# Performance work log

Measured on AMD Instinct MI355X. Metric: run time of the kernel, lower is better.

The kernel has to match this reference:

```python
import jax, jax.numpy as jnp
import numpy as np

N = 50000        # nodes
E = 1600000      # edges
G = 512          # graphs in batch
IN = 128         # in_dim
HID = 32         # hidden_dim
H = 4            # heads in conv1
NEG_SLOPE = 0.2  # PyG GATConv default


def setup_inputs() -> dict:
    key = jax.random.key(0)
    ks = jax.random.split(key, 20)
    s = 0.05
    return {
        "x": jax.random.normal(ks[0], (N, IN), jnp.float32),
        "edge_index": jax.random.randint(ks[1], (2, E), 0, N, dtype=jnp.int64),
        "edge_attr": jax.random.normal(ks[2], (E, 8), jnp.float32),
        "batch": jnp.sort(jax.random.randint(ks[3], (N,), 0, G, dtype=jnp.int64)),
        # conv1: in=IN, out=HID, heads=H, concat=True
        "W1": jax.random.normal(ks[4], (IN, H * HID), jnp.float32) * s,
        "a_src1": jax.random.normal(ks[5], (H, HID), jnp.float32) * s,
        "a_dst1": jax.random.normal(ks[6], (H, HID), jnp.float32) * s,
        "b1": jnp.zeros((H * HID,), jnp.float32),
        # conv2: in=H*HID, out=HID, heads=1, concat=False
        "W2": jax.random.normal(ks[7], (H * HID, HID), jnp.float32) * s,
        "a_src2": jax.random.normal(ks[8], (1, HID), jnp.float32) * s,
        "a_dst2": jax.random.normal(ks[9], (1, HID), jnp.float32) * s,
        "b2": jnp.zeros((HID,), jnp.float32),
        # classifier: HID -> HID//2 -> 1
        "Wc1": jax.random.normal(ks[10], (HID, HID // 2), jnp.float32) * s,
        "bc1": jnp.zeros((HID // 2,), jnp.float32),
        "Wc2": jax.random.normal(ks[11], (HID // 2, 1), jnp.float32) * s,
        "bc2": jnp.zeros((1,), jnp.float32),
    }


def gat_layer(x, src, dst, W, a_src, a_dst, b, heads, ch, concat, n):
    """PyG GATConv (eval mode): linear, edge-gathered additive attention,
    per-destination segment softmax, scatter-add aggregation."""
    h = (x @ W).reshape(n, heads, ch)                       # [N,H,C]
    alpha_s = jnp.sum(h * a_src, axis=-1)                   # [N,H]
    alpha_d = jnp.sum(h * a_dst, axis=-1)                   # [N,H]
    e = jax.nn.leaky_relu(alpha_s[src] + alpha_d[dst], NEG_SLOPE)  # [Etot,H]
    m = jax.lax.stop_gradient(jax.ops.segment_max(e, dst, num_segments=n))
    ex = jnp.exp(e - m[dst])
    den = jax.ops.segment_sum(ex, dst, num_segments=n)      # [N,H]
    alpha = ex / den[dst]                                   # [Etot,H]
    out = jax.ops.segment_sum(alpha[:, :, None] * h[src], dst, num_segments=n)
    out = out.reshape(n, heads * ch) if concat else out.mean(axis=1)
    return out + b


def reference(x, edge_index, edge_attr, batch,
              W1, a_src1, a_dst1, b1,
              W2, a_src2, a_dst2, b2,
              Wc1, bc1, Wc2, bc2):
    # add self-loops (PyG GATConv default)
    loop = jnp.arange(N, dtype=edge_index.dtype)
    src = jnp.concatenate([edge_index[0], loop])
    dst = jnp.concatenate([edge_index[1], loop])

    h = jax.nn.elu(gat_layer(x, src, dst, W1, a_src1, a_dst1, b1, H, HID, True, N))
    h = jax.nn.elu(gat_layer(h, src, dst, W2, a_src2, a_dst2, b2, 1, HID, False, N))

    # global mean pool over graphs
    cnt = jax.ops.segment_sum(jnp.ones((N,), h.dtype), batch, num_segments=G)
    pooled = jax.ops.segment_sum(h, batch, num_segments=G) / cnt[:, None]

    z = jax.nn.relu(pooled @ Wc1 + bc1)
    return (z @ Wc2 + bc2).squeeze(-1)   # [G]
```

## Files before the change

kernel.cpp:

```cpp
#include <hip/hip_runtime.h>
#include <math.h>

#define BUCKET_SHIFT 7
#define BUCKET_NODES (1 << BUCKET_SHIFT)
#define MAX_BUCK 512
#define PART_CHUNK 8192
#define PART_EPT 32

typedef _Float16 half4v __attribute__((ext_vector_type(4)));
typedef _Float16 half8v __attribute__((ext_vector_type(8)));

__device__ __forceinline__ float leaky02(float x){ return x > 0.f ? x : 0.2f * x; }
__device__ __forceinline__ float eluf(float x){ return x > 0.f ? x : expm1f(x); }

__global__ __launch_bounds__(128) void gemm1_kernel(
    const float* __restrict__ x, const float* __restrict__ W,
    const float* __restrict__ a_src, const float* __restrict__ a_dst,
    _Float16* __restrict__ h, float* __restrict__ as_, float* __restrict__ ad_, int n)
{
  const int t = threadIdx.x;
  const int row0 = blockIdx.x * 8;
  __shared__ float xs[8][128];
  __shared__ float sS[8][128];
  __shared__ float sD[8][128];
  for (int idx = t; idx < 8 * 32; idx += 128) {
    int r = idx >> 5, k4 = idx & 31;
    float4 v = (row0 + r < n) ? ((const float4*)x)[(size_t)(row0 + r) * 32 + k4]
                              : make_float4(0.f, 0.f, 0.f, 0.f);
    *(float4*)&xs[r][k4 * 4] = v;
  }
  __syncthreads();
  float acc[8] = {0,0,0,0,0,0,0,0};
  for (int k = 0; k < 128; k += 4) {
    float w0 = W[(k + 0) * 128 + t];
    float w1 = W[(k + 1) * 128 + t];
    float w2 = W[(k + 2) * 128 + t];
    float w3 = W[(k + 3) * 128 + t];
    #pragma unroll
    for (int r = 0; r < 8; ++r) {
      float4 xv = *(const float4*)&xs[r][k];
      acc[r] += xv.x * w0 + xv.y * w1 + xv.z * w2 + xv.w * w3;
    }
  }
  float asv = a_src[t], adv = a_dst[t];
  #pragma unroll
  for (int r = 0; r < 8; ++r) {
    float hv = acc[r];
    if (row0 + r < n) h[(size_t)(row0 + r) * 128 + t] = (_Float16)hv;
    sS[r][t] = hv * asv;
    sD[r][t] = hv * adv;
  }
  __syncthreads();
  if (t < 64) {
    int r = t >> 3, head = t & 3, which = (t >> 2) & 1;
    if (row0 + r < n) {
      const float (*buf)[128] = which ? sD : sS;
      double s = 0;
      for (int cc = 0; cc < 32; ++cc) s += (double)buf[r][head * 32 + cc];
      float* dstp = which ? ad_ : as_;
      dstp[(row0 + r) * 4 + head] = (float)s;
    }
  }
}

__global__ __launch_bounds__(128) void gemm2_kernel(
    const _Float16* __restrict__ x, const float* __restrict__ W,
    const float* __restrict__ a_src, const float* __restrict__ a_dst,
    _Float16* __restrict__ h, float* __restrict__ as_, float* __restrict__ ad_, int n)
{
  const int t = threadIdx.x;
  const int row0 = blockIdx.x * 8;
  __shared__ float xs[8][128];
  __shared__ float sH[8][32];
  for (int idx = t; idx < 8 * 16; idx += 128) {
    int r = idx >> 4, k8 = idx & 15;
    half8v v;
    #pragma unroll
    for (int q = 0; q < 8; ++q) v[q] = (_Float16)0.f;
    if (row0 + r < n) v = ((const half8v*)x)[(size_t)(row0 + r) * 16 + k8];
    #pragma unroll
    for (int q = 0; q < 8; ++q) xs[r][k8 * 8 + q] = (float)v[q];
  }
  __syncthreads();
  int col = t & 31, rp = t >> 5;
  int r0 = rp * 2, r1 = r0 + 1;
  float a0 = 0, a1 = 0;
  for (int k = 0; k < 128; k += 4) {
    float w0 = W[(k + 0) * 32 + col];
    float w1 = W[(k + 1) * 32 + col];
    float w2 = W[(k + 2) * 32 + col];
    float w3 = W[(k + 3) * 32 + col];
    float4 x0 = *(const float4*)&xs[r0][k];
    float4 x1 = *(const float4*)&xs[r1][k];
    a0 += x0.x * w0 + x0.y * w1 + x0.z * w2 + x0.w * w3;
    a1 += x1.x * w0 + x1.y * w1 + x1.z * w2 + x1.w * w3;
  }
  if (row0 + r0 < n) h[(size_t)(row0 + r0) * 32 + col] = (_Float16)a0;
  if (row0 + r1 < n) h[(size_t)(row0 + r1) * 32 + col] = (_Float16)a1;
  sH[r0][col] = a0; sH[r1][col] = a1;
  __syncthreads();
  if (t < 16) {
    int r = t >> 1, which = t & 1;
    if (row0 + r < n) {
      const float* a = which ? a_dst : a_src;
      double s = 0;
      for (int cc = 0; cc < 32; ++cc) s += (double)sH[r][cc] * (double)a[cc];
      (which ? ad_ : as_)[row0 + r] = (float)s;
    }
  }
}

__global__ __launch_bounds__(256) void bucket_hist_kernel(
    const int* __restrict__ dst, int* __restrict__ bucketCount, int E, int K)
{
  __shared__ int hist[MAX_BUCK];
  for (int b = threadIdx.x; b < K; b += 256) hist[b] = 0;
  __syncthreads();
  int cbase = blockIdx.x * PART_CHUNK;
  for (int j = 0; j < PART_EPT; ++j) {
    int e = cbase + j * 256 + threadIdx.x;
    if (e < E) atomicAdd(&hist[dst[e] >> BUCKET_SHIFT], 1);
  }
  __syncthreads();
  for (int b = threadIdx.x; b < K; b += 256)
    if (hist[b]) atomicAdd(&bucketCount[b], hist[b]);
}

__global__ __launch_bounds__(256) void partition_kernel(
    const int* __restrict__ src, const int* __restrict__ dst,
    const int* __restrict__ bucketStart, int* __restrict__ cursorB,
    int2* __restrict__ bucketed, int E, int K)
{
  __shared__ int hist[MAX_BUCK];
  __shared__ int base_s[MAX_BUCK];
  __shared__ int cur[MAX_BUCK];
  for (int b = threadIdx.x; b < K; b += 256) hist[b] = 0;
  __syncthreads();
  int cbase = blockIdx.x * PART_CHUNK;
  for (int j = 0; j < PART_EPT; ++j) {
    int e = cbase + j * 256 + threadIdx.x;
    if (e < E) atomicAdd(&hist[dst[e] >> BUCKET_SHIFT], 1);
  }
  __syncthreads();
  for (int b = threadIdx.x; b < K; b += 256) {
    int c = hist[b];
    base_s[b] = c ? bucketStart[b] + atomicAdd(&cursorB[b], c) : 0;
    cur[b] = 0;
  }
  __syncthreads();
  for (int j = 0; j < PART_EPT; ++j) {
    int e = cbase + j * 256 + threadIdx.x;
    if (e < E) {
      int d = dst[e];
      int b = d >> BUCKET_SHIFT;
      int r = atomicAdd(&cur[b], 1);
      bucketed[base_s[b] + r] = make_int2(src[e], d);
    }
  }
}

__global__ __launch_bounds__(256) void fill_csr_kernel(
    const int2* __restrict__ bucketed, const int* __restrict__ bucketStart,
    int* __restrict__ rowStart, int* __restrict__ col, int n, int E, int K)
{
  int b = blockIdx.x;
  int nodeBase = b << BUCKET_SHIFT;
  int t = threadIdx.x;
  __shared__ int hist[BUCKET_NODES];
  __shared__ int rs[BUCKET_NODES];
  __shared__ int cur[BUCKET_NODES];
  if (t < BUCKET_NODES) hist[t] = 0;
  __syncthreads();
  int bs = bucketStart[b];
  int be = (b + 1 < K) ? bucketStart[b + 1] : E;
  for (int i = bs + t; i < be; i += 256)
    atomicAdd(&hist[bucketed[i].y - nodeBase], 1);
  __syncthreads();
  if (t < BUCKET_NODES) rs[t] = hist[t];
  __syncthreads();
  for (int off = 1; off < BUCKET_NODES; off <<= 1) {
    int v = (t < BUCKET_NODES && t >= off) ? rs[t - off] : 0;
    __syncthreads();
    if (t < BUCKET_NODES) rs[t] += v;
    __syncthreads();
  }
  if (t < BUCKET_NODES) {
    int node = nodeBase + t;
    int excl = bs + rs[t] - hist[t];
    if (node < n) rowStart[node] = excl;
    rs[t] = excl;
    cur[t] = 0;
  }
  if (b == K - 1 && t == 0) rowStart[n] = E;
  __syncthreads();
  for (int i = bs + t; i < be; i += 256) {
    int2 rec = bucketed[i];
    int local = rec.y - nodeBase;
    int pos = rs[local] + atomicAdd(&cur[local], 1);
    col[pos] = rec.x;
  }
}

__global__ __launch_bounds__(256) void gat_aggr_w16_kernel(
    const _Float16* __restrict__ feat,
    const float* __restrict__ as_,
    const float* __restrict__ ad_,
    const int* __restrict__ rowStart,
    const int* __restrict__ col,
    const float* __restrict__ bias,
    _Float16* __restrict__ out, int n)
{
  constexpr int L    = 16;
  constexpr int NPW  = 4;
  constexpr int NPB  = 16;
  constexpr int CHUNK = 16;

  const int t    = threadIdx.x;
  const int wave = t >> 6;
  const int lane = t & 63;
  const int grp  = lane >> 4;
  const int li   = lane & 15;
  const int slot = wave * NPW + grp;
  const int node = blockIdx.x * NPB + slot;
  const int hc   = li >> 2;

  __shared__ int   s_off[NPB][CHUNK + 1];
  __shared__ float s_p[NPB][CHUNK * 4 + 1];

  if (node >= n) return;

  const int beg = rowStart[node];
  const int deg = rowStart[node + 1] - beg;

  const float4 advv = ((const float4*)ad_)[node];
  const float4 asvv = ((const float4*)as_)[node];
  float adv[4] = {advv.x, advv.y, advv.z, advv.w};
  float eself[4];
  eself[0] = leaky02(asvv.x + adv[0]);
  eself[1] = leaky02(asvv.y + adv[1]);
  eself[2] = leaky02(asvv.z + adv[2]);
  eself[3] = leaky02(asvv.w + adv[3]);
  float es = 0.f;
  #pragma unroll
  for (int h = 0; h < 4; ++h) if (h == hc) es = eself[h];
  const float ps = expf(es);

  const char* featc = (const char*)feat + (li << 4);
  const half8v fself = *(const half8v*)(featc + ((size_t)node << 8));
  double acc64[8];
  #pragma unroll
  for (int q = 0; q < 8; ++q) acc64[q] = (double)ps * (double)(float)fself[q];
  double den64 = (double)ps;

  for (int base = 0; base < deg; base += CHUNK) {
    const int cnt = min(CHUNK, deg - base);
    if (li < cnt) {
      int s = col[beg + base + li];
      s_off[slot][li] = s << 8;
      float4 q = ((const float4*)as_)[s];
      s_p[slot][li * 4 + 0] = expf(leaky02(q.x + adv[0]));
      s_p[slot][li * 4 + 1] = expf(leaky02(q.y + adv[1]));
      s_p[slot][li * 4 + 2] = expf(leaky02(q.z + adv[2]));
      s_p[slot][li * 4 + 3] = expf(leaky02(q.w + adv[3]));
    }
    __builtin_amdgcn_wave_barrier();
    float a[8] = {0,0,0,0,0,0,0,0};
    float df = 0.f;
    #pragma unroll 4
    for (int j = 0; j < cnt; ++j) {
      int boff = s_off[slot][j];
      float p = s_p[slot][j * 4 + hc];
      const half8v f = *(const half8v*)(featc + boff);
      #pragma unroll
      for (int q = 0; q < 8; ++q) a[q] += p * (float)f[q];
      df += p;
    }
    __builtin_amdgcn_wave_barrier();
    #pragma unroll
    for (int q = 0; q < 8; ++q) acc64[q] += a[q];
    den64 += df;
  }

  const float4 bv0 = ((const float4*)bias)[2 * li];
  const float4 bv1 = ((const float4*)bias)[2 * li + 1];
  const float bb[8] = {bv0.x, bv0.y, bv0.z, bv0.w, bv1.x, bv1.y, bv1.z, bv1.w};
  const double inv = 1.0 / den64;
  half8v ov;
  #pragma unroll
  for (int q = 0; q < 8; ++q)
    ov[q] = (_Float16)eluf((float)(acc64[q] * inv) + bb[q]);
  *(half8v*)((char*)out + ((size_t)node << 8) + (li << 4)) = ov;
}

template<int CTOT, int H>
__global__ __launch_bounds__(256) void gat_aggr3_kernel(
    const _Float16* __restrict__ feat,
    const float* __restrict__ as_,
    const float* __restrict__ ad_,
    const int* __restrict__ rowStart,
    const int* __restrict__ col,
    const float* __restrict__ bias,
    float* __restrict__ out, int n)
{
  constexpr int L    = CTOT / 4;
  constexpr int NPW  = 64 / L;
  constexpr int NPB  = 4 * NPW;
  constexpr int CH   = CTOT / H;
  constexpr int CHUNK = L;

  const int t    = threadIdx.x;
  const int wave = t >> 6;
  const int lane = t & 63;
  const int grp  = lane / L;
  const int li   = lane % L;
  const int slot = wave * NPW + grp;
  const int node = blockIdx.x * NPB + slot;
  const int hc   = (4 * li) / CH;

  __shared__ int   s_off[NPB][CHUNK + 1];
  __shared__ float s_p[NPB][CHUNK * H + 1];

  if (node >= n) return;

  const int beg = rowStart[node];
  const int deg = rowStart[node + 1] - beg;

  float adv[H], eself[H];
  #pragma unroll
  for (int h = 0; h < H; ++h) adv[h] = ad_[node * H + h];
  #pragma unroll
  for (int h = 0; h < H; ++h) eself[h] = leaky02(as_[node * H + h] + adv[h]);

  float es = 0.f;
  #pragma unroll
  for (int h = 0; h < H; ++h) if (h == hc) es = eself[h];
  const float ps = expf(es);

  const half4v fself = *(const half4v*)(feat + (size_t)node * CTOT + 4 * li);
  double acc64[4];
  acc64[0] = (double)ps * (double)(float)fself.x;
  acc64[1] = (double)ps * (double)(float)fself.y;
  acc64[2] = (double)ps * (double)(float)fself.z;
  acc64[3] = (double)ps * (double)(float)fself.w;
  double den64 = (double)ps;

  for (int base = 0; base < deg; base += CHUNK) {
    const int cnt = min(CHUNK, deg - base);
    if (li < cnt) {
      int s = col[beg + base + li];
      s_off[slot][li] = s * CTOT;
      if constexpr (H == 4) {
        float4 q = ((const float4*)as_)[s];
        s_p[slot][li * 4 + 0] = expf(leaky02(q.x + adv[0]));
        s_p[slot][li * 4 + 1] = expf(leaky02(q.y + adv[1]));
        s_p[slot][li * 4 + 2] = expf(leaky02(q.z + adv[2]));
        s_p[slot][li * 4 + 3] = expf(leaky02(q.w + adv[3]));
      } else {
        s_p[slot][li] = expf(leaky02(as_[s] + adv[0]));
      }
    }
    __builtin_amdgcn_wave_barrier();
    float a0 = 0.f, a1 = 0.f, a2 = 0.f, a3 = 0.f, df = 0.f;
    #pragma unroll 8
    for (int j = 0; j < cnt; ++j) {
      int off = s_off[slot][j];
      float p = (H == 4) ? s_p[slot][j * 4 + hc] : s_p[slot][j];
      const half4v f = *(const half4v*)(feat + off + 4 * li);
      a0 += p * (float)f.x; a1 += p * (float)f.y;
      a2 += p * (float)f.z; a3 += p * (float)f.w;
      df += p;
    }
    __builtin_amdgcn_wave_barrier();
    acc64[0] += a0; acc64[1] += a1; acc64[2] += a2; acc64[3] += a3;
    den64 += df;
  }

  const float4 bv = *(const float4*)(bias + 4 * li);
  float4 o;
  o.x = eluf((float)(acc64[0] / den64) + bv.x);
  o.y = eluf((float)(acc64[1] / den64) + bv.y);
  o.z = eluf((float)(acc64[2] / den64) + bv.z);
  o.w = eluf((float)(acc64[3] / den64) + bv.w);
  *(float4*)(out + (size_t)node * CTOT + 4 * li) = o;
}

__global__ __launch_bounds__(256) void pool_kernel(const float* __restrict__ act2,
    const int* __restrict__ batch, float* __restrict__ pooled,
    float* __restrict__ cnt, int n)
{
  int t = threadIdx.x;
  int c = t & 31, r = t >> 5;
  int n0 = blockIdx.x * 64 + r * 8;
  float run = 0.f; int gcur = -1; int len = 0;
  for (int i = 0; i < 8; ++i) {
    int nd = n0 + i;
    if (nd >= n) break;
    int gb = batch[nd];
    if (gb != gcur) {
      if (gcur >= 0) {
        atomicAdd(&pooled[gcur * 32 + c], run);
        if (c == 0) atomicAdd(&cnt[gcur], (float)len);
      }
      gcur = gb; run = 0.f; len = 0;
    }
    run += act2[(size_t)nd * 32 + c];
    len++;
  }
  if (gcur >= 0) {
    atomicAdd(&pooled[gcur * 32 + c], run);
    if (c == 0) atomicAdd(&cnt[gcur], (float)len);
  }
}

__global__ void classifier_kernel(const float* __restrict__ pooled, const float* __restrict__ cnt,
    const float* __restrict__ Wc1, const float* __restrict__ bc1,
    const float* __restrict__ Wc2, const float* __restrict__ bc2,
    float* __restrict__ outp, int g_total)
{
  int g = blockIdx.x * blockDim.x + threadIdx.x;
  if (g < g_total) {
    float inv = 1.0f / cnt[g];
    float pm[32];
    for (int c = 0; c < 32; ++c) pm[c] = pooled[g * 32 + c] * inv;
    double o = (double)bc2[0];
    for (int j = 0; j < 16; ++j) {
      double z = (double)bc1[j];
      for (int c = 0; c < 32; ++c) z += (double)pm[c] * (double)Wc1[c * 16 + j];
      float zr = (float)z;
      zr = zr > 0.f ? zr : 0.f;
      o += (double)zr * (double)Wc2[j];
    }
    outp[g] = (float)o;
  }
}

extern "C" void kernel_launch(void* const* d_in, const int* in_sizes, int n_in,
                              void* d_out, int out_size, void* d_ws, size_t ws_size,
                              hipStream_t stream)
{
  const float* x      = (const float*)d_in[0];
  const int*   ei     = (const int*)d_in[1];
  const int*   batch  = (const int*)d_in[3];
  const float* W1     = (const float*)d_in[4];
  const float* a_src1 = (const float*)d_in[5];
  const float* a_dst1 = (const float*)d_in[6];
  const float* b1     = (const float*)d_in[7];
  const float* W2     = (const float*)d_in[8];
  const float* a_src2 = (const float*)d_in[9];
  const float* a_dst2 = (const float*)d_in[10];
  const float* b2     = (const float*)d_in[11];
  const float* Wc1    = (const float*)d_in[12];
  const float* bc1    = (const float*)d_in[13];
  const float* Wc2    = (const float*)d_in[14];
  const float* bc2    = (const float*)d_in[15];

  const int N = in_sizes[0] / 128;
  const int E = in_sizes[1] / 2;
  const int G = out_size;

  const int* srcv = ei;
  const int* dstv = ei + E;

  char* ws = (char*)d_ws;
  size_t off = 0;
  auto alloc = [&](size_t bytes) -> void* {
    void* p = ws + off;
    off += (bytes + 255) & ~(size_t)255;
    return p;
  };
  _Float16* h1   = (_Float16*)alloc((size_t)N * 128 * 2);
  _Float16* act1 = (_Float16*)alloc((size_t)N * 128 * 2);
  _Float16* h2   = (_Float16*)alloc((size_t)N * 32 * 2);
  float* act2  = (float*)alloc((size_t)N * 32 * 4);
  float* as1   = (float*)alloc((size_t)N * 4 * 4);
  float* ad1   = (float*)alloc((size_t)N * 4 * 4);
  float* as2   = (float*)alloc((size_t)N * 4);
  float* ad2   = (float*)alloc((size_t)N * 4);
  int*   rowStart = (int*)alloc((size_t)(N + 1) * 4);
  int*   colv     = (int*)alloc((size_t)E * 4);
  int*   bucketCount = (int*)alloc((size_t)MAX_BUCK * 4);
  int*   cursorB     = (int*)alloc((size_t)MAX_BUCK * 4);
  int2*  bucketed    = (int2*)alloc((size_t)E * 8);
  float* pooled   = (float*)alloc((size_t)G * 32 * 4);
  float* cntG     = (float*)alloc((size_t)G * 4);

  const int K = (N + BUCKET_NODES - 1) >> BUCKET_SHIFT;

  hipMemsetAsync(bucketCount, 0, (size_t)K * 4, stream);
  hipMemsetAsync(cursorB,     0, (size_t)K * 4, stream);
  hipMemsetAsync(pooled, 0, (size_t)G * 32 * 4, stream);
  hipMemsetAsync(cntG,   0, (size_t)G * 4, stream);

  int pb = (E + PART_CHUNK - 1) / PART_CHUNK;
  bucket_hist_kernel<<<pb, 256, 0, stream>>>(dstv, bucketCount, E, K);
  {
    extern __global__ void scan_offsets_kernel(int*, int);
  }
  void(0);
  {
    extern const int __dummy;
  }
  extern __global__ void scan_offsets_kernel(int* __restrict__, int);
  scan_offsets_kernel<<<1, 256, 0, stream>>>(bucketCount, K);
  partition_kernel<<<pb, 256, 0, stream>>>(srcv, dstv, bucketCount, cursorB, bucketed, E, K);
  fill_csr_kernel<<<K, 256, 0, stream>>>(bucketed, bucketCount, rowStart, colv, N, E, K);

  gemm1_kernel<<<(N + 7) / 8, 128, 0, stream>>>(x, W1, a_src1, a_dst1, h1, as1, ad1, N);
  gat_aggr_w16_kernel<<<(N + 15) / 16, 256, 0, stream>>>(h1, as1, ad1, rowStart, colv, b1, act1, N);

  gemm2_kernel<<<(N + 7) / 8, 128, 0, stream>>>(act1, W2, a_src2, a_dst2, h2, as2, ad2, N);
  gat_aggr3_kernel<32, 1><<<(N + 31) / 32, 256, 0, stream>>>(h2, as2, ad2, rowStart, colv, b2, act2, N);

  pool_kernel<<<(N + 63) / 64, 256, 0, stream>>>(act2, batch, pooled, cntG, N);
  classifier_kernel<<<(G + 255) / 256, 256, 0, stream>>>(pooled, cntG, Wc1, bc1, Wc2, bc2,
                                                         (float*)d_out, G);
}

__global__ __launch_bounds__(256) void scan_offsets_kernel(int* __restrict__ partial, int nb) {
  __shared__ int s[256];
  __shared__ int carry_s;
  int t = threadIdx.x;
  if (t == 0) carry_s = 0;
  __syncthreads();
  for (int b = 0; b < nb; b += 256) {
    int v = (b + t < nb) ? partial[b + t] : 0;
    s[t] = v;
    __syncthreads();
    for (int off = 1; off < 256; off <<= 1) {
      int x = (t >= off) ? s[t - off] : 0;
      __syncthreads();
      s[t] += x;
      __syncthreads();
    }
    int incl = s[t];
    int carry = carry_s;
    if (b + t < nb) partial[b + t] = carry + incl - v;
    __syncthreads();
    if (t == 255) carry_s = carry + incl;
    __syncthreads();
  }
}
```

Measured before the change: 398.3 us.

## Split layer-1 aggregation per head with head-major features and packed bucket records

gemm1 now writes features and attention logits in head-major layout ([head][node][32]), so layer-1 aggregation runs as four independent 32-channel slices on a 2D grid, sharing one generic slice kernel with layer 2. Each per-head gathered row is 64 bytes, which shrinks the random-access working set per pass and should improve cache hit rates. The slice kernel prefetches the next chunk's column indices and source logits into registers and fully unrolls 16 gathers for full chunks. The CSR bucketed records are packed into 32 bits (src<<7 | local dst), halving partition traffic. The cost is that the column list and rowStart are re-read four times, once per head, and the packing assumes src fits in 25 bits.

```diff
diff --git a/kernel.cpp b/kernel.cpp
--- a/kernel.cpp
+++ b/kernel.cpp
@@ -42,23 +42,25 @@
       acc[r] += xv.x * w0 + xv.y * w1 + xv.z * w2 + xv.w * w3;
     }
   }
+  const int head = t >> 5, cc = t & 31;
   float asv = a_src[t], adv = a_dst[t];
   #pragma unroll
   for (int r = 0; r < 8; ++r) {
     float hv = acc[r];
-    if (row0 + r < n) h[(size_t)(row0 + r) * 128 + t] = (_Float16)hv;
+    if (row0 + r < n)
+      h[((size_t)head * n + (row0 + r)) * 32 + cc] = (_Float16)hv;
     sS[r][t] = hv * asv;
     sD[r][t] = hv * adv;
   }
   __syncthreads();
   if (t < 64) {
-    int r = t >> 3, head = t & 3, which = (t >> 2) & 1;
+    int r = t >> 3, hd = t & 3, which = (t >> 2) & 1;
     if (row0 + r < n) {
       const float (*buf)[128] = which ? sD : sS;
       double s = 0;
-      for (int cc = 0; cc < 32; ++cc) s += (double)buf[r][head * 32 + cc];
+      for (int c2 = 0; c2 < 32; ++c2) s += (double)buf[r][hd * 32 + c2];
       float* dstp = which ? ad_ : as_;
-      dstp[(row0 + r) * 4 + head] = (float)s;
+      dstp[(size_t)hd * n + (row0 + r)] = (float)s;
     }
   }
 }
@@ -126,10 +128,35 @@
     if (hist[b]) atomicAdd(&bucketCount[b], hist[b]);
 }
 
+__global__ __launch_bounds__(256) void scan_offsets_kernel(int* __restrict__ partial, int nb) {
+  __shared__ int s[256];
+  __shared__ int carry_s;
+  int t = threadIdx.x;
+  if (t == 0) carry_s = 0;
+  __syncthreads();
+  for (int b = 0; b < nb; b += 256) {
+    int v = (b + t < nb) ? partial[b + t] : 0;
+    s[t] = v;
+    __syncthreads();
+    for (int off = 1; off < 256; off <<= 1) {
+      int x = (t >= off) ? s[t - off] : 0;
+      __syncthreads();
+      s[t] += x;
+      __syncthreads();
+    }
+    int incl = s[t];
+    int carry = carry_s;
+    if (b + t < nb) partial[b + t] = carry + incl - v;
+    __syncthreads();
+    if (t == 255) carry_s = carry + incl;
+    __syncthreads();
+  }
+}
+
 __global__ __launch_bounds__(256) void partition_kernel(
     const int* __restrict__ src, const int* __restrict__ dst,
     const int* __restrict__ bucketStart, int* __restrict__ cursorB,
-    int2* __restrict__ bucketed, int E, int K)
+    unsigned int* __restrict__ bucketed, int E, int K)
 {
   __shared__ int hist[MAX_BUCK];
   __shared__ int base_s[MAX_BUCK];
@@ -154,13 +181,14 @@
       int d = dst[e];
       int b = d >> BUCKET_SHIFT;
       int r = atomicAdd(&cur[b], 1);
-      bucketed[base_s[b] + r] = make_int2(src[e], d);
+      bucketed[base_s[b] + r] =
+          ((unsigned int)src[e] << BUCKET_SHIFT) | (unsigned int)(d & (BUCKET_NODES - 1));
     }
   }
 }
 
 __global__ __launch_bounds__(256) void fill_csr_kernel(
-    const int2* __restrict__ bucketed, const int* __restrict__ bucketStart,
+    const unsigned int* __restrict__ bucketed, const int* __restrict__ bucketStart,
     int* __restrict__ rowStart, int* __restrict__ col, int n, int E, int K)
 {
   int b = blockIdx.x;
@@ -174,7 +202,7 @@
   int bs = bucketStart[b];
   int be = (b + 1 < K) ? bucketStart[b + 1] : E;
   for (int i = bs + t; i < be; i += 256)
-    atomicAdd(&hist[bucketed[i].y - nodeBase], 1);
+    atomicAdd(&hist[bucketed[i] & (BUCKET_NODES - 1)], 1);
   __syncthreads();
   if (t < BUCKET_NODES) rs[t] = hist[t];
   __syncthreads();
@@ -194,149 +222,54 @@
   if (b == K - 1 && t == 0) rowStart[n] = E;
   __syncthreads();
   for (int i = bs + t; i < be; i += 256) {
-    int2 rec = bucketed[i];
-    int local = rec.y - nodeBase;
+    unsigned int rec = bucketed[i];
+    int local = rec & (BUCKET_NODES - 1);
     int pos = rs[local] + atomicAdd(&cur[local], 1);
-    col[pos] = rec.x;
-  }
-}
-
-__global__ __launch_bounds__(256) void gat_aggr_w16_kernel(
+    col[pos] = (int)(rec >> BUCKET_SHIFT);
+  }
+}
+
+template<typename OUT_T>
+__global__ __launch_bounds__(256) void gat_slice_kernel(
     const _Float16* __restrict__ feat,
     const float* __restrict__ as_,
     const float* __restrict__ ad_,
     const int* __restrict__ rowStart,
     const int* __restrict__ col,
     const float* __restrict__ bias,
-    _Float16* __restrict__ out, int n)
-{
-  constexpr int L    = 16;
-  constexpr int NPW  = 4;
-  constexpr int NPB  = 16;
+    OUT_T* __restrict__ out,
+    int n, int outStride)
+{
+  constexpr int L = 8;
+  constexpr int NPW = 8;
+  constexpr int NPB = 32;
   constexpr int CHUNK = 16;
 
   const int t    = threadIdx.x;
   const int wave = t >> 6;
   const int lane = t & 63;
-  const int grp  = lane >> 4;
-  const int li   = lane & 15;
+  const int grp  = lane >> 3;
+  const int li   = lane & 7;
   const int slot = wave * NPW + grp;
   const int node = blockIdx.x * NPB + slot;
-  const int hc   = li >> 2;
-
-  __shared__ int   s_off[NPB][CHUNK + 1];
-  __shared__ float s_p[NPB][CHUNK * 4 + 1];
+  const int s    = blockIdx.y;
+
+  __shared__ int   s_off[NPB][CHUNK];
+  __shared__ float s_p[NPB][CHUNK];
 
   if (node >= n) return;
+
+  const _Float16* featS = feat + (size_t)s * n * 32;
+  const float*    asS   = as_ + (size_t)s * n;
 
   const int beg = rowStart[node];
   const int deg = rowStart[node + 1] - beg;
 
-  const float4 advv = ((const float4*)ad_)[node];
-  const float4 asvv = ((const float4*)as_)[node];
-  float adv[4] = {advv.x, advv.y, advv.z, advv.w};
-  float eself[4];
-  eself[0] = leaky02(asvv.x + adv[0]);
-  eself[1] = leaky02(asvv.y + adv[1]);
-  eself[2] = leaky02(asvv.z + adv[2]);
-  eself[3] = leaky02(asvv.w + adv[3]);
-  float es = 0.f;
-  #pragma unroll
-  for (int h = 0; h < 4; ++h) if (h == hc) es = eself[h];
-  const float ps = expf(es);
-
-  const char* featc = (const char*)feat + (li << 4);
-  const half8v fself = *(const half8v*)(featc + ((size_t)node << 8));
-  double acc64[8];
-  #pragma unroll
-  for (int q = 0; q < 8; ++q) acc64[q] = (double)ps * (double)(float)fself[q];
-  double den64 = (double)ps;
-
-  for (int base = 0; base < deg; base += CHUNK) {
-    const int cnt = min(CHUNK, deg - base);
-    if (li < cnt) {
-      int s = col[beg + base + li];
-      s_off[slot][li] = s << 8;
-      float4 q = ((const float4*)as_)[s];
-      s_p[slot][li * 4 + 0] = expf(leaky02(q.x + adv[0]));
-      s_p[slot][li * 4 + 1] = expf(leaky02(q.y + adv[1]));
-      s_p[slot][li * 4 + 2] = expf(leaky02(q.z + adv[2]));
-      s_p[slot][li * 4 + 3] = expf(leaky02(q.w + adv[3]));
-    }
-    __builtin_amdgcn_wave_barrier();
-    float a[8] = {0,0,0,0,0,0,0,0};
-    float df = 0.f;
-    #pragma unroll 4
-    for (int j = 0; j < cnt; ++j) {
-      int boff = s_off[slot][j];
-      float p = s_p[slot][j * 4 + hc];
-      const half8v f = *(const half8v*)(featc + boff);
-      #pragma unroll
-      for (int q = 0; q < 8; ++q) a[q] += p * (float)f[q];
-      df += p;
-    }
-    __builtin_amdgcn_wave_barrier();
-    #pragma unroll
-    for (int q = 0; q < 8; ++q) acc64[q] += a[q];
-    den64 += df;
-  }
-
-  const float4 bv0 = ((const float4*)bias)[2 * li];
-  const float4 bv1 = ((const float4*)bias)[2 * li + 1];
-  const float bb[8] = {bv0.x, bv0.y, bv0.z, bv0.w, bv1.x, bv1.y, bv1.z, bv1.w};
-  const double inv = 1.0 / den64;
-  half8v ov;
-  #pragma unroll
-  for (int q = 0; q < 8; ++q)
-    ov[q] = (_Float16)eluf((float)(acc64[q] * inv) + bb[q]);
-  *(half8v*)((char*)out + ((size_t)node << 8) + (li << 4)) = ov;
-}
-
-template<int CTOT, int H>
-__global__ __launch_bounds__(256) void gat_aggr3_kernel(
-    const _Float16* __restrict__ feat,
-    const float* __restrict__ as_,
-    const float* __restrict__ ad_,
-    const int* __restrict__ rowStart,
-    const int* __restrict__ col,
-    const float* __restrict__ bias,
-    float* __restrict__ out, int n)
-{
-  constexpr int L    = CTOT / 4;
-  constexpr int NPW  = 64 / L;
-  constexpr int NPB  = 4 * NPW;
-  constexpr int CH   = CTOT / H;
-  constexpr int CHUNK = L;
-
-  const int t    = threadIdx.x;
-  const int wave = t >> 6;
-  const int lane = t & 63;
-  const int grp  = lane / L;
-  const int li   = lane % L;
-  const int slot = wave * NPW + grp;
-  const int node = blockIdx.x * NPB + slot;
-  const int hc   = (4 * li) / CH;
-
-  __shared__ int   s_off[NPB][CHUNK + 1];
-  __shared__ float s_p[NPB][CHUNK * H + 1];
-
-  if (node >= n) return;
-
-  const int beg = rowStart[node];
-  const int deg = rowStart[node + 1] - beg;
-
-  float adv[H], eself[H];
-  #pragma unroll
-  for (int h = 0; h < H; ++h) adv[h] = ad_[node * H + h];
-  #pragma unroll
-  for (int h = 0; h < H; ++h) eself[h] = leaky02(as_[node * H + h] + adv[h]);
-
-  float es = 0.f;
-  #pragma unroll
-  for (int h = 0; h < H; ++h) if (h == hc) es = eself[h];
-  const float ps = expf(es);
-
-  const half4v fself = *(const half4v*)(feat + (size_t)node * CTOT + 4 * li);
+  const float adv = ad_[(size_t)s * n + node];
+  const float ps  = expf(leaky02(asS[node] + adv));
+
+  const char* featc = (const char*)featS + (li << 3);
+  const half4v fself = *(const half4v*)(featc + ((size_t)node << 6));
   double acc64[4];
   acc64[0] = (double)ps * (double)(float)fself.x;
   acc64[1] = (double)ps * (double)(float)fself.y;
@@ -344,44 +277,98 @@
   acc64[3] = (double)ps * (double)(float)fself.w;
   double den64 = (double)ps;
 
-  for (int base = 0; base < deg; base += CHUNK) {
-    const int cnt = min(CHUNK, deg - base);
-    if (li < cnt) {
-      int s = col[beg + base + li];
-      s_off[slot][li] = s * CTOT;
-      if constexpr (H == 4) {
-        float4 q = ((const float4*)as_)[s];
-        s_p[slot][li * 4 + 0] = expf(leaky02(q.x + adv[0]));
-        s_p[slot][li * 4 + 1] = expf(leaky02(q.y + adv[1]));
-        s_p[slot][li * 4 + 2] = expf(leaky02(q.z + adv[2]));
-        s_p[slot][li * 4 + 3] = expf(leaky02(q.w + adv[3]));
-      } else {
-        s_p[slot][li] = expf(leaky02(as_[s] + adv[0]));
+  int   st_s0 = 0, st_s1 = 0;
+  float st_q0 = 0.f, st_q1 = 0.f;
+
+  const int nch = (deg + CHUNK - 1) / CHUNK;
+  if (nch > 0) {
+    int cnt0 = min(CHUNK, deg);
+    if (li < cnt0)     { st_s0 = col[beg + li];     st_q0 = asS[st_s0]; }
+    if (li + 8 < cnt0) { st_s1 = col[beg + li + 8]; st_q1 = asS[st_s1]; }
+  }
+
+  for (int c = 0; c < nch; ++c) {
+    const int base = c * CHUNK;
+    const int cnt  = min(CHUNK, deg - base);
+    if (li < cnt)     { s_off[slot][li]     = st_s0 << 6; s_p[slot][li]     = expf(leaky02(st_q0 + adv)); }
+    if (li + 8 < cnt) { s_off[slot][li + 8] = st_s1 << 6; s_p[slot][li + 8] = expf(leaky02(st_q1 + adv)); }
+    __builtin_amdgcn_wave_barrier();
+    const int nbase = base + CHUNK;
+    if (nbase < deg) {
+      int ncnt = min(CHUNK, deg - nbase);
+      if (li < ncnt)     { st_s0 = col[beg + nbase + li];     st_q0 = asS[st_s0]; }
+      if (li + 8 < ncnt) { st_s1 = col[beg + nbase + li + 8]; st_q1 = asS[st_s1]; }
+    }
+    float a0 = 0.f, a1 = 0.f, a2 = 0.f, a3 = 0.f, df = 0.f;
+    if (cnt == CHUNK) {
+      int4 o0 = *(const int4*)&s_off[slot][0];
+      int4 o1 = *(const int4*)&s_off[slot][4];
+      int4 o2 = *(const int4*)&s_off[slot][8];
+      int4 o3 = *(const int4*)&s_off[slot][12];
+      half4v r[16];
+      r[0]  = *(const half4v*)(featc + o0.x);
+      r[1]  = *(const half4v*)(featc + o0.y);
+      r[2]  = *(const half4v*)(featc + o0.z);
+      r[3]  = *(const half4v*)(featc + o0.w);
+      r[4]  = *(const half4v*)(featc + o1.x);
+      r[5]  = *(const half4v*)(featc + o1.y);
+      r[6]  = *(const half4v*)(featc + o1.z);
+      r[7]  = *(const half4v*)(featc + o1.w);
+      r[8]  = *(const half4v*)(featc + o2.x);
+      r[9]  = *(const half4v*)(featc + o2.y);
+      r[10] = *(const half4v*)(featc + o2.z);
+      r[11] = *(const half4v*)(featc + o2.w);
+      r[12] = *(const half4v*)(featc + o3.x);
+      r[13] = *(const half4v*)(featc + o3.y);
+      r[14] = *(const half4v*)(featc + o3.z);
+      r[15] = *(const half4v*)(featc + o3.w);
+      float4 p0 = *(const float4*)&s_p[slot][0];
+      float4 p1 = *(const float4*)&s_p[slot][4];
+      float4 p2 = *(const float4*)&s_p[slot][8];
+      float4 p3 = *(const float4*)&s_p[slot][12];
+      const float pv[16] = {p0.x,p0.y,p0.z,p0.w, p1.x,p1.y,p1.z,p1.w,
+                            p2.x,p2.y,p2.z,p2.w, p3.x,p3.y,p3.z,p3.w};
+      #pragma unroll
+      for (int j = 0; j < 16; ++j) {
+        float p = pv[j];
+        a0 += p * (float)r[j].x; a1 += p * (float)r[j].y;
+        a2 += p * (float)r[j].z; a3 += p * (float)r[j].w;
+        df += p;
       }
-    }
-    __builtin_amdgcn_wave_barrier();
-    float a0 = 0.f, a1 = 0.f, a2 = 0.f, a3 = 0.f, df = 0.f;
-    #pragma unroll 8
-    for (int j = 0; j < cnt; ++j) {
-      int off = s_off[slot][j];
-      float p = (H == 4) ? s_p[slot][j * 4 + hc] : s_p[slot][j];
-      const half4v f = *(const half4v*)(feat + off + 4 * li);
-      a0 += p * (float)f.x; a1 += p * (float)f.y;
-      a2 += p * (float)f.z; a3 += p * (float)f.w;
-      df += p;
+    } else {
+      #pragma unroll 4
+      for (int j = 0; j < cnt; ++j) {
+        int off = s_off[slot][j];
+        float p = s_p[slot][j];
+        const half4v f = *(const half4v*)(featc + off);
+        a0 += p * (float)f.x; a1 += p * (float)f.y;
+        a2 += p * (float)f.z; a3 += p * (float)f.w;
+        df += p;
+      }
     }
     __builtin_amdgcn_wave_barrier();
     acc64[0] += a0; acc64[1] += a1; acc64[2] += a2; acc64[3] += a3;
     den64 += df;
   }
 
-  const float4 bv = *(const float4*)(bias + 4 * li);
-  float4 o;
-  o.x = eluf((float)(acc64[0] / den64) + bv.x);
-  o.y = eluf((float)(acc64[1] / den64) + bv.y);
-  o.z = eluf((float)(acc64[2] / den64) + bv.z);
-  o.w = eluf((float)(acc64[3] / den64) + bv.w);
-  *(float4*)(out + (size_t)node * CTOT + 4 * li) = o;
+  const double inv = 1.0 / den64;
+  const float4 bv = *(const float4*)(bias + s * 32 + 4 * li);
+  OUT_T* op = out + (size_t)node * outStride + s * 32 + 4 * li;
+  if constexpr (sizeof(OUT_T) == 2) {
+    half4v ov;
+    ov.x = (_Float16)eluf((float)(acc64[0] * inv) + bv.x);
+    ov.y = (_Float16)eluf((float)(acc64[1] * inv) + bv.y);
+    ov.z = (_Float16)eluf((float)(acc64[2] * inv) + bv.z);
+    ov.w = (_Float16)eluf((float)(acc64[3] * inv) + bv.w);
+    *(half4v*)op = ov;
+  } else {
+    float4 o;
+    o.x = eluf((float)(acc64[0] * inv) + bv.x);
+    o.y = eluf((float)(acc64[1] * inv) + bv.y);
+    o.z = eluf((float)(acc64[2] * inv) + bv.z);
+    o.w = eluf((float)(acc64[3] * inv) + bv.w);
+    *(float4*)op = o;
+  }
 }
 
 __global__ __launch_bounds__(256) void pool_kernel(const float* __restrict__ act2,
@@ -480,7 +467,7 @@
   int*   colv     = (int*)alloc((size_t)E * 4);
   int*   bucketCount = (int*)alloc((size_t)MAX_BUCK * 4);
   int*   cursorB     = (int*)alloc((size_t)MAX_BUCK * 4);
-  int2*  bucketed    = (int2*)alloc((size_t)E * 8);
+  unsigned int* bucketed = (unsigned int*)alloc((size_t)E * 4);
   float* pooled   = (float*)alloc((size_t)G * 32 * 4);
   float* cntG     = (float*)alloc((size_t)G * 4);
 
@@ -493,50 +480,21 @@
 
   int pb = (E + PART_CHUNK - 1) / PART_CHUNK;
   bucket_hist_kernel<<<pb, 256, 0, stream>>>(dstv, bucketCount, E, K);
-  {
-    extern __global__ void scan_offsets_kernel(int*, int);
-  }
-  void(0);
-  {
-    extern const int __dummy;
-  }
-  extern __global__ void scan_offsets_kernel(int* __restrict__, int);
   scan_offsets_kernel<<<1, 256, 0, stream>>>(bucketCount, K);
   partition_kernel<<<pb, 256, 0, stream>>>(srcv, dstv, bucketCount, cursorB, bucketed, E, K);
   fill_csr_kernel<<<K, 256, 0, stream>>>(bucketed, bucketCount, rowStart, colv, N, E, K);
 
   gemm1_kernel<<<(N + 7) / 8, 128, 0, stream>>>(x, W1, a_src1, a_dst1, h1, as1, ad1, N);
-  gat_aggr_w16_kernel<<<(N + 15) / 16, 256, 0, stream>>>(h1, as1, ad1, rowStart, colv, b1, act1, N);
+  dim3 g1((N + 31) / 32, 4);
+  gat_slice_kernel<_Float16><<<g1, 256, 0, stream>>>(h1, as1, ad1, rowStart, colv, b1,
+                                                     act1, N, 128);
 
   gemm2_kernel<<<(N + 7) / 8, 128, 0, stream>>>(act1, W2, a_src2, a_dst2, h2, as2, ad2, N);
-  gat_aggr3_kernel<32, 1><<<(N + 31) / 32, 256, 0, stream>>>(h2, as2, ad2, rowStart, colv, b2, act2, N);
+  dim3 g2((N + 31) / 32, 1);
+  gat_slice_kernel<float><<<g2, 256, 0, stream>>>(h2, as2, ad2, rowStart, colv, b2,
+                                                  act2, N, 32);
 
   pool_kernel<<<(N + 63) / 64, 256, 0, stream>>>(act2, batch, pooled, cntG, N);
   classifier_kernel<<<(G + 255) / 256, 256, 0, stream>>>(pooled, cntG, Wc1, bc1, Wc2, bc2,
                                                          (float*)d_out, G);
 }
-
-__global__ __launch_bounds__(256) void scan_offsets_kernel(int* __restrict__ partial, int nb) {
-  __shared__ int s[256];
-  __shared__ int carry_s;
-  int t = threadIdx.x;
-  if (t == 0) carry_s = 0;
-  __syncthreads();
-  for (int b = 0; b < nb; b += 256) {
-    int v = (b + t < nb) ? partial[b + t] : 0;
-    s[t] = v;
-    __syncthreads();
-    for (int off = 1; off < 256; off <<= 1) {
-      int x = (t >= off) ? s[t - off] : 0;
-      __syncthreads();
-      s[t] += x;
-      __syncthreads();
-    }
-    int incl = s[t];
-    int carry = carry_s;
-    if (b + t < nb) partial[b + t] = carry + incl - v;
-    __syncthreads();
-    if (t == 255) carry_s = carry + incl;
-    __syncthreads();
-  }
-}
```

After: 418.7 us. +5.1%, slower.
